# Performance work log

Measured on AMD Instinct MI355X. Metric: run time of the kernel, lower is better.

The kernel has to match this reference:

```python
import jax, jax.numpy as jnp
import numpy as np

N = 4096
IN_F = 256
HEADS = 8
OUT_F = 64  # per-head dim
NEG_BIG = -9e15


def setup_inputs() -> dict:
    key = jax.random.key(0)
    k1, k2, k3, k4 = jax.random.split(key, 4)
    x = jax.random.normal(k1, (N, IN_F), dtype=jnp.float32)
    adj = jax.random.randint(k2, (N, N), 0, 2, dtype=jnp.int32)
    # linear weight (no bias): torch Linear(in, heads*out) -> store as [in, heads*out]
    lim_w = float(np.sqrt(6.0 / (IN_F + HEADS * OUT_F)))
    W = jax.random.uniform(k3, (IN_F, HEADS * OUT_F), minval=-lim_w, maxval=lim_w, dtype=jnp.float32)
    # attn param [1, heads, 2*out], xavier_uniform
    lim_a = float(np.sqrt(6.0 / (HEADS + 2 * OUT_F)))
    attn = jax.random.uniform(k4, (1, HEADS, 2 * OUT_F), minval=-lim_a, maxval=lim_a, dtype=jnp.float32)
    return {"x": x, "adj": adj, "W": W, "attn": attn}


def reference(x, adj, W, attn):
    n = x.shape[0]
    H = attn.shape[1]
    D = attn.shape[2] // 2
    h = (x @ W).reshape(n, H, D)                       # [N, H, D]
    a_src = attn[0, :, :D]                             # [H, D]
    a_dst = attn[0, :, D:]                             # [H, D]
    # separable GAT score: e[i, j, h] = a_src.h_i + a_dst.h_j
    s_src = jnp.einsum('nhd,hd->nh', h, a_src)         # [N, H]
    s_dst = jnp.einsum('nhd,hd->nh', h, a_dst)         # [N, H]
    e = s_src[:, None, :] + s_dst[None, :, :]          # [N, N, H]
    e = jnp.where(adj[:, :, None] > 0, e, jnp.float32(NEG_BIG))
    attention = jax.nn.softmax(e, axis=1)              # softmax over neighbor dim j
    h_prime = jnp.einsum('ijh,jhd->ihd', attention, h)  # [N, H, D]
    return h_prime.reshape(n, H * D)
```

## Files before the change

### kernel.cpp

```cpp
#include <hip/hip_runtime.h>
#include <hip/hip_bf16.h>
#include <stdint.h>

typedef __attribute__((ext_vector_type(4))) float  f32x4;
typedef __attribute__((ext_vector_type(8))) short  s16x8;
typedef __attribute__((ext_vector_type(4))) int    i32x4;
typedef __attribute__((ext_vector_type(8))) unsigned short u16x8;

#define NN 4096
#define GT_LD 4096
#define NUM_STRIDE (4096 * 512)

__device__ __forceinline__ unsigned short f2bf(float f) {
  uint32_t u = __builtin_bit_cast(uint32_t, f);
  u += 0x7FFF + ((u >> 16) & 1);
  return (unsigned short)(u >> 16);
}

__device__ __forceinline__ void gload_lds16(const void* g, void* l) {
  __builtin_amdgcn_global_load_lds(
      (const __attribute__((address_space(1))) unsigned int*)g,
      (__attribute__((address_space(3))) unsigned int*)l, 16, 0, 0);
}

__global__ __launch_bounds__(512) void k_small(const float* __restrict__ x,
                                               const float* __restrict__ W,
                                               unsigned short* __restrict__ xb,
                                               unsigned short* __restrict__ wt) {
  int bid = blockIdx.x;
  if (bid < 512) {
    int t = bid * 512 + threadIdx.x;
    f32x4 v = ((const f32x4*)x)[t];
    uint64_t r = (uint64_t)f2bf(v.x) | ((uint64_t)f2bf(v.y) << 16) |
                 ((uint64_t)f2bf(v.z) << 32) | ((uint64_t)f2bf(v.w) << 48);
    ((uint64_t*)xb)[t] = r;
  } else {
    int t = (bid - 512) * 512 + threadIdx.x;
    int c = t >> 8, k = t & 255;
    wt[t] = f2bf(W[k * 512 + c]);
  }
}

__global__ __launch_bounds__(512) void k_fat(const int* __restrict__ adj,
                                             unsigned short* __restrict__ ab,
                                             const unsigned short* __restrict__ xb,
                                             const unsigned short* __restrict__ wt,
                                             const float* __restrict__ attn,
                                             unsigned short* __restrict__ gt) {
  __shared__ unsigned short lx[16 * 256];
  __shared__ unsigned short lw[512 * 64];

  if (blockIdx.x >= 256) {
    int t = (blockIdx.x - 256) * 512 + threadIdx.x;
    const i32x4* p = (const i32x4*)adj;
    i32x4 v0 = p[2 * t], v1 = p[2 * t + 1];
    u16x8 r;
    r[0] = v0.x ? 0x3F80 : 0; r[1] = v0.y ? 0x3F80 : 0;
    r[2] = v0.z ? 0x3F80 : 0; r[3] = v0.w ? 0x3F80 : 0;
    r[4] = v1.x ? 0x3F80 : 0; r[5] = v1.y ? 0x3F80 : 0;
    r[6] = v1.z ? 0x3F80 : 0; r[7] = v1.w ? 0x3F80 : 0;
    ((u16x8*)ab)[t] = r;
    return;
  }

  const int tid = threadIdx.x;
  const int lane = tid & 63;
  const int h = tid >> 6;
  const int l15 = lane & 15, lg = lane >> 4;
  const int j0 = blockIdx.x * 16;

  {
    int L = tid * 16;
    int row = L >> 9, b = L & 511;
    int sb = b ^ ((row & 7) << 4);
    gload_lds16((const char*)xb + (j0 + row) * 512 + sb, (char*)lx + L);
  }

  f32x4 acc[4] = {};
  for (int kc = 0; kc < 4; ++kc) {
#pragma unroll
    for (int i = 0; i < 8; ++i) {
      int L = (i * 512 + tid) * 16;
      int c = L >> 7, b = L & 127;
      int sb = b ^ ((c & 7) << 4);
      gload_lds16((const char*)wt + c * 512 + kc * 128 + sb, (char*)lw + L);
    }
    asm volatile("s_waitcnt vmcnt(0)");
    __syncthreads();
#pragma unroll
    for (int kk = 0; kk < 2; ++kk) {
      int kby = kk * 64 + lg * 16;
      s16x8 a = *(const s16x8*)((const char*)lx + l15 * 512 +
                                ((kc * 128 + kby) ^ ((l15 & 7) << 4)));
#pragma unroll
      for (int n = 0; n < 4; ++n) {
        int c = h * 64 + n * 16 + l15;
        s16x8 b = *(const s16x8*)((const char*)lw + c * 128 + (kby ^ ((c & 7) << 4)));
        acc[n] = __builtin_amdgcn_mfma_f32_16x16x32_bf16(a, b, acc[n], 0, 0, 0);
      }
    }
    __syncthreads();
  }

  float adv[4];
#pragma unroll
  for (int n = 0; n < 4; ++n) adv[n] = attn[h * 128 + 64 + n * 16 + l15];
#pragma unroll
  for (int r = 0; r < 4; ++r) {
    float p = acc[0][r] * adv[0] + acc[1][r] * adv[1] +
              acc[2][r] * adv[2] + acc[3][r] * adv[3];
#pragma unroll
    for (int m = 1; m < 16; m <<= 1) p += __shfl_xor(p, m);
    float w = expf(p);
    int node = j0 + lg * 4 + r;
#pragma unroll
    for (int n = 0; n < 4; ++n) {
      int c = h * 64 + n * 16 + l15;
      gt[c * GT_LD + node] = f2bf(acc[n][r] * w);
    }
    if (l15 == 0) gt[(512 + h) * GT_LD + node] = f2bf(w);
  }
}

__global__ __launch_bounds__(256, 4) void k_gemm(const unsigned short* __restrict__ A,
                                                 const unsigned short* __restrict__ GT,
                                                 float* __restrict__ out,
                                                 float* __restrict__ numx,
                                                 float* __restrict__ den,
                                                 int klen) {
  __shared__ unsigned short lA[128 * 64];
  __shared__ unsigned short lB[128 * 64];
  const int tid = threadIdx.x;
  const int lane = tid & 63, wid = tid >> 6;
  const int wr = wid >> 1, wc = wid & 1;
  const int l15 = lane & 15, lg = lane >> 4;

  int g = blockIdx.x;
  int swz = (g & 7) * 20 + (g >> 3);
  int bx = swz / 5, by = swz % 5;
  const int row0 = bx * 128, c0 = by * 128;

  const int s = blockIdx.y;
  float* num = (s == 0) ? out : (numx + (s - 1) * NUM_STRIDE);
  float* dens = den + s * (4096 * 8);

  const char* Abase = (const char*)A + row0 * 8192 + (long)s * klen * 2;
  const char* Bbase = (const char*)GT + c0 * 8192 + (long)s * klen * 2;

  auto stage = [&](const char* base, unsigned short* dst, int kt) {
#pragma unroll
    for (int i = 0; i < 4; ++i) {
      int L = (i * 256 + tid) * 16;
      int r = L >> 7, b = L & 127;
      int sb = b ^ ((r & 7) << 4);
      gload_lds16(base + r * 8192 + kt * 128 + sb, (char*)dst + L);
    }
  };

  f32x4 acc[4][4] = {};
  const int NKT = klen >> 6;

  for (int kt = 0; kt < NKT; ++kt) {
    stage(Abase, lA, kt);
    stage(Bbase, lB, kt);
    __syncthreads();
#pragma unroll
    for (int kk = 0; kk < 2; ++kk) {
      int kby = kk * 64 + lg * 16;
      s16x8 a[4], b[4];
#pragma unroll
      for (int m = 0; m < 4; ++m) {
        int r = wr * 64 + m * 16 + l15;
        a[m] = *(const s16x8*)((const char*)lA + r * 128 + (kby ^ ((r & 7) << 4)));
      }
#pragma unroll
      for (int n = 0; n < 4; ++n) {
        int c = wc * 64 + n * 16 + l15;
        b[n] = *(const s16x8*)((const char*)lB + c * 128 + (kby ^ ((c & 7) << 4)));
      }
#pragma unroll
      for (int m = 0; m < 4; ++m)
#pragma unroll
        for (int n = 0; n < 4; ++n)
          acc[m][n] = __builtin_amdgcn_mfma_f32_16x16x32_bf16(a[m], b[n], acc[m][n], 0, 0, 0);
    }
    __syncthreads();
  }

#pragma unroll
  for (int m = 0; m < 4; ++m)
#pragma unroll
    for (int n = 0; n < 4; ++n) {
      int c = c0 + wc * 64 + n * 16 + l15;
#pragma unroll
      for (int r = 0; r < 4; ++r) {
        int i = row0 + wr * 64 + m * 16 + lg * 4 + r;
        float v = acc[m][n][r];
        if (c < 512) num[i * 512 + c] = v;
        else if (c < 520) dens[i * 8 + (c - 512)] = v;
      }
    }
}

__global__ __launch_bounds__(256) void k_final(float* __restrict__ out,
                                               const float* __restrict__ numx,
                                               const float* __restrict__ den,
                                               int S) {
  int t = blockIdx.x * 256 + threadIdx.x;
  int i = t >> 7, h = (t >> 4) & 7;
  f32x4 v = ((const f32x4*)out)[t];
  float d = den[i * 8 + h];
  for (int s = 1; s < S; ++s) {
    f32x4 u = ((const f32x4*)(numx + (s - 1) * NUM_STRIDE))[t];
    v.x += u.x; v.y += u.y; v.z += u.z; v.w += u.w;
    d += den[s * 4096 * 8 + i * 8 + h];
  }
  v.x /= d; v.y /= d; v.z /= d; v.w /= d;
  ((f32x4*)out)[t] = v;
}

extern "C" void kernel_launch(void* const* d_in, const int* in_sizes, int n_in,
                              void* d_out, int out_size, void* d_ws, size_t ws_size,
                              hipStream_t stream) {
  const float* x    = (const float*)d_in[0];
  const int*   adj  = (const int*)d_in[1];
  const float* W    = (const float*)d_in[2];
  const float* attn = (const float*)d_in[3];
  float* out = (float*)d_out;
  char* ws = (char*)d_ws;

  unsigned short* Ab  = (unsigned short*)(ws);
  unsigned short* GTp = (unsigned short*)(ws + 33554432);
  unsigned short* XB  = (unsigned short*)(ws + 38273024);
  unsigned short* WT  = (unsigned short*)(ws + 40370176);
  float*          DEN = (float*)(ws + 40632320);
  float*          NUMX = (float*)(ws + 41156608);

  int S = 1;
  if (ws_size >= 41156608ull + 3ull * NUM_STRIDE * 4 + 65536) S = 4;
  else if (ws_size >= 41156608ull + 1ull * NUM_STRIDE * 4 + 65536) S = 2;

  k_small<<<768, 512, 0, stream>>>(x, W, XB, WT);
  k_fat  <<<4352, 512, 0, stream>>>(adj, Ab, XB, WT, attn, GTp);
  dim3 ggrid(160, S);
  k_gemm <<<ggrid, 256, 0, stream>>>(Ab, GTp, out, NUMX, DEN, 4096 / S);
  k_final<<<2048, 256, 0, stream>>>(out, NUMX, DEN, S);
}
```

Measured before the change: 67.43 us.

## Pack adjacency into bitmask and expand to bf16 tiles inside GEMM

The adjacency conversion now produces a 1-bit-per-entry mask using wave ballots instead of a full bf16 matrix. The GEMM reads 32-bit mask words per row and expands them into bf16 ones and zeros directly in shared memory, prefetching the next word. This cuts the workspace write in the conversion pass and the A-operand global read in the GEMM from 32 MB to 2 MB. In exchange the GEMM does ALU expansion and LDS stores every k-step, and its launch bound drops to 3 blocks per CU.

```diff
diff --git a/kernel.cpp b/kernel.cpp
--- a/kernel.cpp
+++ b/kernel.cpp
@@ -5,7 +5,7 @@
 typedef __attribute__((ext_vector_type(4))) float  f32x4;
 typedef __attribute__((ext_vector_type(8))) short  s16x8;
 typedef __attribute__((ext_vector_type(4))) int    i32x4;
-typedef __attribute__((ext_vector_type(8))) unsigned short u16x8;
+typedef __attribute__((ext_vector_type(4))) unsigned int u32x4;
 
 #define NN 4096
 #define GT_LD 4096
@@ -42,7 +42,7 @@
 }
 
 __global__ __launch_bounds__(512) void k_fat(const int* __restrict__ adj,
-                                             unsigned short* __restrict__ ab,
+                                             unsigned int* __restrict__ bits,
                                              const unsigned short* __restrict__ xb,
                                              const unsigned short* __restrict__ wt,
                                              const float* __restrict__ attn,
@@ -51,15 +51,16 @@
   __shared__ unsigned short lw[512 * 64];
 
   if (blockIdx.x >= 256) {
-    int t = (blockIdx.x - 256) * 512 + threadIdx.x;
-    const i32x4* p = (const i32x4*)adj;
-    i32x4 v0 = p[2 * t], v1 = p[2 * t + 1];
-    u16x8 r;
-    r[0] = v0.x ? 0x3F80 : 0; r[1] = v0.y ? 0x3F80 : 0;
-    r[2] = v0.z ? 0x3F80 : 0; r[3] = v0.w ? 0x3F80 : 0;
-    r[4] = v1.x ? 0x3F80 : 0; r[5] = v1.y ? 0x3F80 : 0;
-    r[6] = v1.z ? 0x3F80 : 0; r[7] = v1.w ? 0x3F80 : 0;
-    ((u16x8*)ab)[t] = r;
+    int row = blockIdx.x - 256;
+    int w = threadIdx.x >> 6, lane = threadIdx.x & 63;
+    const int* ap = adj + row * 4096 + w * 512;
+    unsigned long long* bp = (unsigned long long*)(bits + row * 128) + w * 8;
+#pragma unroll
+    for (int k = 0; k < 8; ++k) {
+      int v = ap[k * 64 + lane];
+      unsigned long long mask = __ballot(v != 0);
+      if (lane == 0) bp[k] = mask;
+    }
     return;
   }
 
@@ -122,7 +123,7 @@
   }
 }
 
-__global__ __launch_bounds__(256, 4) void k_gemm(const unsigned short* __restrict__ A,
+__global__ __launch_bounds__(256, 3) void k_gemm(const unsigned int* __restrict__ bits,
                                                  const unsigned short* __restrict__ GT,
                                                  float* __restrict__ out,
                                                  float* __restrict__ numx,
@@ -144,34 +145,51 @@
   float* num = (s == 0) ? out : (numx + (s - 1) * NUM_STRIDE);
   float* dens = den + s * (4096 * 8);
 
-  const char* Abase = (const char*)A + row0 * 8192 + (long)s * klen * 2;
+  const int r = tid >> 1, hf = tid & 1;
+  const unsigned int* bitrow = bits + (row0 + r) * 128 + s * (klen >> 5) + hf;
+
   const char* Bbase = (const char*)GT + c0 * 8192 + (long)s * klen * 2;
 
-  auto stage = [&](const char* base, unsigned short* dst, int kt) {
+  auto stageB = [&](int kt) {
 #pragma unroll
     for (int i = 0; i < 4; ++i) {
       int L = (i * 256 + tid) * 16;
-      int r = L >> 7, b = L & 127;
-      int sb = b ^ ((r & 7) << 4);
-      gload_lds16(base + r * 8192 + kt * 128 + sb, (char*)dst + L);
+      int rr = L >> 7, b = L & 127;
+      int sb = b ^ ((rr & 7) << 4);
+      gload_lds16(Bbase + rr * 8192 + kt * 128 + sb, (char*)lB + L);
+    }
+  };
+  auto expandA = [&](uint32_t m) {
+#pragma unroll
+    for (int q = 0; q < 4; ++q) {
+      u32x4 w;
+#pragma unroll
+      for (int d = 0; d < 4; ++d) {
+        int b = q * 8 + d * 2;
+        w[d] = ((m >> b) & 1u) * 0x3F80u + ((m >> (b + 1)) & 1u) * 0x3F800000u;
+      }
+      int byte = (hf * 64 + q * 16) ^ ((r & 7) << 4);
+      *(u32x4*)((char*)lA + r * 128 + byte) = w;
     }
   };
 
   f32x4 acc[4][4] = {};
   const int NKT = klen >> 6;
 
+  uint32_t m = bitrow[0];
   for (int kt = 0; kt < NKT; ++kt) {
-    stage(Abase, lA, kt);
-    stage(Bbase, lB, kt);
+    uint32_t m2 = (kt < NKT - 1) ? bitrow[(kt + 1) * 2] : 0;
+    stageB(kt);
+    expandA(m);
     __syncthreads();
 #pragma unroll
     for (int kk = 0; kk < 2; ++kk) {
       int kby = kk * 64 + lg * 16;
       s16x8 a[4], b[4];
 #pragma unroll
-      for (int m = 0; m < 4; ++m) {
-        int r = wr * 64 + m * 16 + l15;
-        a[m] = *(const s16x8*)((const char*)lA + r * 128 + (kby ^ ((r & 7) << 4)));
+      for (int mm = 0; mm < 4; ++mm) {
+        int rr = wr * 64 + mm * 16 + l15;
+        a[mm] = *(const s16x8*)((const char*)lA + rr * 128 + (kby ^ ((rr & 7) << 4)));
       }
 #pragma unroll
       for (int n = 0; n < 4; ++n) {
@@ -179,23 +197,24 @@
         b[n] = *(const s16x8*)((const char*)lB + c * 128 + (kby ^ ((c & 7) << 4)));
       }
 #pragma unroll
-      for (int m = 0; m < 4; ++m)
+      for (int mm = 0; mm < 4; ++mm)
 #pragma unroll
         for (int n = 0; n < 4; ++n)
-          acc[m][n] = __builtin_amdgcn_mfma_f32_16x16x32_bf16(a[m], b[n], acc[m][n], 0, 0, 0);
-    }
-    __syncthreads();
-  }
-
-#pragma unroll
-  for (int m = 0; m < 4; ++m)
+          acc[mm][n] = __builtin_amdgcn_mfma_f32_16x16x32_bf16(a[mm], b[n], acc[mm][n], 0, 0, 0);
+    }
+    m = m2;
+    __syncthreads();
+  }
+
+#pragma unroll
+  for (int mm = 0; mm < 4; ++mm)
 #pragma unroll
     for (int n = 0; n < 4; ++n) {
       int c = c0 + wc * 64 + n * 16 + l15;
 #pragma unroll
-      for (int r = 0; r < 4; ++r) {
-        int i = row0 + wr * 64 + m * 16 + lg * 4 + r;
-        float v = acc[m][n][r];
+      for (int rr = 0; rr < 4; ++rr) {
+        int i = row0 + wr * 64 + mm * 16 + lg * 4 + rr;
+        float v = acc[mm][n][rr];
         if (c < 512) num[i * 512 + c] = v;
         else if (c < 520) dens[i * 8 + (c - 512)] = v;
       }
@@ -229,20 +248,20 @@
   float* out = (float*)d_out;
   char* ws = (char*)d_ws;
 
-  unsigned short* Ab  = (unsigned short*)(ws);
-  unsigned short* GTp = (unsigned short*)(ws + 33554432);
-  unsigned short* XB  = (unsigned short*)(ws + 38273024);
-  unsigned short* WT  = (unsigned short*)(ws + 40370176);
-  float*          DEN = (float*)(ws + 40632320);
-  float*          NUMX = (float*)(ws + 41156608);
+  unsigned int*   BITS = (unsigned int*)(ws);
+  unsigned short* GTp  = (unsigned short*)(ws + 2097152);
+  unsigned short* XB   = (unsigned short*)(ws + 6815744);
+  unsigned short* WT   = (unsigned short*)(ws + 8912896);
+  float*          DEN  = (float*)(ws + 9175040);
+  float*          NUMX = (float*)(ws + 9699328);
 
   int S = 1;
-  if (ws_size >= 41156608ull + 3ull * NUM_STRIDE * 4 + 65536) S = 4;
-  else if (ws_size >= 41156608ull + 1ull * NUM_STRIDE * 4 + 65536) S = 2;
+  if (ws_size >= 9699328ull + 3ull * NUM_STRIDE * 4 + 65536) S = 4;
+  else if (ws_size >= 9699328ull + 1ull * NUM_STRIDE * 4 + 65536) S = 2;
 
   k_small<<<768, 512, 0, stream>>>(x, W, XB, WT);
-  k_fat  <<<4352, 512, 0, stream>>>(adj, Ab, XB, WT, attn, GTp);
+  k_fat  <<<4352, 512, 0, stream>>>(adj, BITS, XB, WT, attn, GTp);
   dim3 ggrid(160, S);
-  k_gemm <<<ggrid, 256, 0, stream>>>(Ab, GTp, out, NUMX, DEN, 4096 / S);
+  k_gemm <<<ggrid, 256, 0, stream>>>(BITS, GTp, out, NUMX, DEN, 4096 / S);
   k_final<<<2048, 256, 0, stream>>>(out, NUMX, DEN, S);
 }
```

Measured after the change: 82.43 us. 1.22x slower.
